# Kernel optimization log

Measured on AMD Instinct MI355X. Metric: run time of the kernel, lower is better.

The kernel has to match this reference:

```python
import jax, jax.numpy as jnp
import numpy as np

EMBED_DIM = 1024
NUM_HEADS = 16
PROJ_DIM = EMBED_DIM // NUM_HEADS


def setup_inputs() -> dict:
    key = jax.random.key(0)
    ks = jax.random.split(key, 11)
    B, S, D = 2, 2048, EMBED_DIM
    scale = 1.0 / np.sqrt(D)
    inp = {
        'q': jax.random.normal(ks[0], (B, S, D), jnp.float32),
        'k': jax.random.normal(ks[1], (B, S, D), jnp.float32),
        'v': jax.random.normal(ks[2], (B, S, D), jnp.float32),
        'Wq': jax.random.normal(ks[3], (D, D), jnp.float32) * scale,
        'bq': jnp.zeros((D,), jnp.float32),
        'Wk': jax.random.normal(ks[4], (D, D), jnp.float32) * scale,
        'bk': jnp.zeros((D,), jnp.float32),
        'Wv': jax.random.normal(ks[5], (D, D), jnp.float32) * scale,
        'bv': jnp.zeros((D,), jnp.float32),
        'Wo': jax.random.normal(ks[6], (D, D), jnp.float32) * scale,
        'bo': jnp.zeros((D,), jnp.float32),
        'use_causal_mask': 1,
    }
    return inp


def _split_heads(x, B):
    # [B, S, D] -> [B, H, S, Pd]
    return x.reshape(B, -1, NUM_HEADS, PROJ_DIM).transpose(0, 2, 1, 3)


def reference(q, k, v, Wq, bq, Wk, bk, Wv, bv, Wo, bo, use_causal_mask):
    B, S, D = q.shape
    qh = _split_heads(q @ Wq + bq, B)
    kh = _split_heads(k @ Wk + bk, B)
    vh = _split_heads(v @ Wv + bv, B)
    # scaled dot-product attention; scores [B, H, S, S]
    logits = jnp.einsum('bhqd,bhkd->bhqk', qh, kh) / jnp.sqrt(
        jnp.asarray(PROJ_DIM, jnp.float32))
    if use_causal_mask:
        # faithful to source: logits += log(tril * 1e-9 + 1e-9)
        tril = jnp.tril(jnp.ones((S, S), dtype=logits.dtype))
        logits = logits + jnp.log(tril * 1e-9 + 1e-9)
    attn = jax.nn.softmax(logits, axis=-1)
    out = jnp.einsum('bhqk,bhkd->bhqd', attn, vh)
    out = out.transpose(0, 2, 1, 3).reshape(B, S, D)
    return out @ Wo + bo
```

## Files before the change

### kernel.cpp

```cpp
#include <hip/hip_runtime.h>
#include <hip/hip_bf16.h>
#include <stdint.h>

#define EMBED 1024
#define NH    16
#define PD    64
#define BATCH 2
#define SEQ   2048

typedef unsigned short u16;
typedef __attribute__((ext_vector_type(8))) short bf16x8;
typedef __attribute__((ext_vector_type(4))) float f32x4;

#define WAITALL() __builtin_amdgcn_s_waitcnt(0)

__device__ __forceinline__ float b2f(u16 x) {
  unsigned u = ((unsigned)x) << 16;
  return __builtin_bit_cast(float, u);
}
__device__ __forceinline__ u16 cvtb(float x) {
  __bf16 h = (__bf16)x;
  return __builtin_bit_cast(u16, h);
}
__device__ __forceinline__ float loadIn(const void* p, size_t i, int isf32) {
  return isf32 ? ((const float*)p)[i] : b2f(((const u16*)p)[i]);
}
__device__ __forceinline__ void async16(const void* g, void* l) {
  __builtin_amdgcn_global_load_lds((const __attribute__((address_space(1))) void*)g,
                                   (__attribute__((address_space(3))) void*)l,
                                   16, 0, 0);
}
__device__ __forceinline__ int detect_f32(const void* q) {
  unsigned w0 = ((const unsigned*)q)[threadIdx.x & 63];
  unsigned e = (w0 >> 7) & 0xffu;
  unsigned long long m = __ballot(e >= 110 && e <= 135);
  return (__popcll(m) < 32) ? 1 : 0;
}

__global__ __launch_bounds__(256) void conv_fused(
    const void* q, const void* k, const void* v,
    const void* Wq, const void* Wk, const void* Wv, const void* Wo,
    u16* qb, u16* kb, u16* vb, u16* WT_all) {
  __shared__ float sh[64][65];
  const int isf32 = detect_f32(q);

  if (blockIdx.y < 3) {
    size_t i = ((size_t)blockIdx.x * 256 + threadIdx.x) * 8;
    const void* src = (blockIdx.y == 0) ? q : (blockIdx.y == 1) ? k : v;
    u16* dst = (blockIdx.y == 0) ? qb : (blockIdx.y == 1) ? kb : vb;
    u16 tmp[8];
    if (isf32) {
      const float* s = (const float*)src + i;
      float4 a = *(const float4*)s;
      float4 b = *(const float4*)(s + 4);
      tmp[0] = cvtb(a.x); tmp[1] = cvtb(a.y); tmp[2] = cvtb(a.z); tmp[3] = cvtb(a.w);
      tmp[4] = cvtb(b.x); tmp[5] = cvtb(b.y); tmp[6] = cvtb(b.z); tmp[7] = cvtb(b.w);
    } else {
      const uint4 r = *(const uint4*)((const u16*)src + i);
      *(uint4*)tmp = r;
    }
    *(uint4*)(dst + i) = *(uint4*)tmp;
    return;
  }

  if (blockIdx.x >= 1024) return;
  const int z = blockIdx.x >> 8;
  const int xy = blockIdx.x & 255;
  const int bx = xy & 15, by = xy >> 4;
  const void* W = (z == 0) ? Wq : (z == 1) ? Wk : (z == 2) ? Wv : Wo;
  u16* WT = WT_all + (size_t)z * EMBED * EMBED;
  int r0 = by * 64, c0 = bx * 64;
  int col = threadIdx.x & 63;
  int rb  = threadIdx.x >> 6;
#pragma unroll
  for (int i = 0; i < 16; i++) {
    int row = i * 4 + rb;
    sh[row][col] = loadIn(W, (size_t)(r0 + row) * EMBED + c0 + col, isf32);
  }
  __syncthreads();
#pragma unroll
  for (int i = 0; i < 16; i++) {
    int row = i * 4 + rb;
    WT[(size_t)(c0 + row) * EMBED + r0 + col] = cvtb(sh[col][row]);
  }
}

__device__ __forceinline__ void gemm_stage(const u16* __restrict__ A,
                                           const u16* __restrict__ Bt,
                                           int tm, int tn, int kt,
                                           u16* As, u16* Bs, int tid) {
#pragma unroll
  for (int i = 0; i < 4; i++) {
    int c = i * 256 + tid;
    int row = c >> 3;
    int col = ((c & 7) << 3) ^ ((row & 7) << 3);
    async16(A + (size_t)(tm + row) * EMBED + kt + col, As + c * 8);
    async16(Bt + (size_t)(tn + row) * EMBED + kt + col, Bs + c * 8);
  }
}

__device__ __forceinline__ void gemm_compute(const u16* As, const u16* Bs,
                                             int wm, int wn, int l15, int quad,
                                             int rbx, f32x4 acc[4][4]) {
#pragma unroll
  for (int ks = 0; ks < 64; ks += 32) {
    int ko = (ks + quad * 8) ^ rbx;
    bf16x8 af[4], bf[4];
#pragma unroll
    for (int mt = 0; mt < 4; mt++)
      af[mt] = *(const bf16x8*)(As + (wm + mt * 16 + l15) * 64 + ko);
#pragma unroll
    for (int nt = 0; nt < 4; nt++)
      bf[nt] = *(const bf16x8*)(Bs + (wn + nt * 16 + l15) * 64 + ko);
#pragma unroll
    for (int mt = 0; mt < 4; mt++)
#pragma unroll
      for (int nt = 0; nt < 4; nt++)
        acc[mt][nt] = __builtin_amdgcn_mfma_f32_16x16x32_bf16(
            af[mt], bf[nt], acc[mt][nt], 0, 0, 0);
  }
}

__global__ __launch_bounds__(512, 2) void qkv_gemm(
    const u16* qb, const u16* kb, const u16* vb, const u16* wts,
    const void* bq, const void* bk, const void* bv,
    u16* Qh, u16* Kh, u16* Vt, const void* qorig) {
  __shared__ __align__(16) u16 lds[4 * 256 * 64];
  const int isf32 = detect_f32(qorig);

  const int lid = blockIdx.x;
  const int mhi = lid & 7;
  const int mlo = (lid >> 3) & 1;
  const int vx = (lid >> 4) & 3;
  const int z = lid >> 6;
  const int vm = mhi * 2 + mlo;
  const int tm = vm * 256, tn = vx * 256;

  const u16* A = (z == 0) ? qb : (z == 1) ? kb : vb;
  const u16* Bt = wts + (size_t)z * EMBED * EMBED;
  const void* bias = (z == 0) ? bq : (z == 1) ? bk : bv;

  const int tid = threadIdx.x, lane = tid & 63, wv = tid >> 6;
  const int wm = (wv >> 2) * 128, wn = (wv & 3) * 64;
  const int l15 = lane & 15, quad = lane >> 4;
  const int rbx = (lane & 7) << 3;

  f32x4 acc[8][4];
  f32x4 zz = {0.f, 0.f, 0.f, 0.f};
#pragma unroll
  for (int i = 0; i < 8; i++)
#pragma unroll
    for (int j = 0; j < 4; j++) acc[i][j] = zz;

#define QKV_STAGE(kt_, As_, Bs_)                                              \
  {                                                                           \
    _Pragma("unroll") for (int i = 0; i < 4; i++) {                           \
      int c = i * 512 + tid;                                                  \
      int row = c >> 3;                                                       \
      int col = ((c & 7) << 3) ^ ((row & 7) << 3);                            \
      async16(A + (size_t)(tm + row) * EMBED + (kt_) + col, (As_) + c * 8);   \
      async16(Bt + (size_t)(tn + row) * EMBED + (kt_) + col, (Bs_) + c * 8);  \
    }                                                                         \
  }

  QKV_STAGE(0, lds, lds + 16384);
  WAITALL();
  __syncthreads();
  for (int kt = 0; kt < EMBED; kt += 64) {
    const int cur = (kt >> 6) & 1;
    const u16* Asc = lds + cur * 32768;
    const u16* Bsc = Asc + 16384;
    if (kt + 64 < EMBED)
      QKV_STAGE(kt + 64, lds + (cur ^ 1) * 32768, lds + (cur ^ 1) * 32768 + 16384);
#pragma unroll
    for (int ks = 0; ks < 64; ks += 32) {
      int ko = (ks + quad * 8) ^ rbx;
      bf16x8 af[8], bf[4];
#pragma unroll
      for (int mt = 0; mt < 8; mt++)
        af[mt] = *(const bf16x8*)(Asc + (wm + mt * 16 + l15) * 64 + ko);
#pragma unroll
      for (int nt = 0; nt < 4; nt++)
        bf[nt] = *(const bf16x8*)(Bsc + (wn + nt * 16 + l15) * 64 + ko);
#pragma unroll
      for (int mt = 0; mt < 8; mt++)
#pragma unroll
        for (int nt = 0; nt < 4; nt++)
          acc[mt][nt] = __builtin_amdgcn_mfma_f32_16x16x32_bf16(
              af[mt], bf[nt], acc[mt][nt], 0, 0, 0);
    }
    WAITALL();
    __syncthreads();
  }
#undef QKV_STAGE

  int rbase = tm + wm + (quad << 2);
  int cbase = tn + wn + l15;
  if (z < 2) {
    u16* dst = (z == 0) ? Qh : Kh;
#pragma unroll
    for (int mt = 0; mt < 8; mt++)
#pragma unroll
      for (int nt = 0; nt < 4; nt++) {
        int col = cbase + nt * 16;
        float bv_ = loadIn(bias, col, isf32);
        int h = col >> 6, p = col & 63;
#pragma unroll
        for (int j = 0; j < 4; j++) {
          int row = rbase + mt * 16 + j;
          int b = row >> 11, s = row & 2047;
          dst[(((size_t)(b * NH + h) * SEQ) + s) * PD + p] =
              cvtb(acc[mt][nt][j] + bv_);
        }
      }
  } else {
#pragma unroll
    for (int mt = 0; mt < 8; mt++)
#pragma unroll
      for (int nt = 0; nt < 4; nt++) {
        int col = cbase + nt * 16;
        float bv_ = loadIn(bias, col, isf32);
        int h = col >> 6, p = col & 63;
        int row0 = rbase + mt * 16;
        int b = row0 >> 11, s0 = row0 & 2047;
        int beta = s0 >> 5, w = s0 & 31;
        int pos = (beta << 5) + (((w >> 2) & 3) << 3) + ((w >> 4) << 2);
        ushort4 pk;
        pk.x = cvtb(acc[mt][nt][0] + bv_);
        pk.y = cvtb(acc[mt][nt][1] + bv_);
        pk.z = cvtb(acc[mt][nt][2] + bv_);
        pk.w = cvtb(acc[mt][nt][3] + bv_);
        *(ushort4*)(Vt + ((size_t)(b * NH + h) * PD + p) * SEQ + pos) = pk;
      }
  }
}

__global__ __launch_bounds__(256, 4) void attn(const u16* __restrict__ Qh,
                                               const u16* __restrict__ Kh,
                                               const u16* __restrict__ Vt,
                                               u16* __restrict__ O,
                                               const int* __restrict__ maskflag) {
  __shared__ __align__(16) u16 sh[5 * 64 * 64];
  u16* const Vbase = sh + 3 * 4096;
  u16* const Qs    = sh + 2 * 4096;

  const int lid = blockIdx.x + (blockIdx.y << 5);
  const int xcd = lid & 7, j = lid >> 3;
  const int bh = (xcd << 2) | (j & 3);
  const int qt = (j >> 2) * 64;

  const int tid = threadIdx.x, lane = tid & 63, wv = tid >> 6;
  const int qh = wv & 1;
  const int kh = wv >> 1;
  const int l15 = lane & 15, quad = lane >> 4;
  const int rbx = (lane & 7) << 3;
  const size_t head = (size_t)bh * SEQ * PD;
  const bool causal = (maskflag[0] != 0);
  const float C = 0.18033688011112042f;

  const int c0 = tid, c1 = 256 + tid;
  const int r0 = c0 >> 3, r1 = c1 >> 3;
  const int x0 = ((c0 & 7) << 3) ^ ((r0 & 7) << 3);
  const int x1 = ((c1 & 7) << 3) ^ ((r1 & 7) << 3);

  async16(Qh + head + (size_t)(qt + r0) * PD + x0, Qs + c0 * 8);
  async16(Qh + head + (size_t)(qt + r1) * PD + x1, Qs + c1 * 8);
  async16(Kh + head + (size_t)r0 * PD + x0, sh + c0 * 8);
  async16(Kh + head + (size_t)r1 * PD + x1, sh + c1 * 8);
  async16(Vt + head + (size_t)r0 * SEQ + x0, Vbase + c0 * 8);
  async16(Vt + head + (size_t)r1 * SEQ + x1, Vbase + c1 * 8);
  async16(Kh + head + (size_t)(64 + r0) * PD + x0, sh + 4096 + c0 * 8);
  async16(Kh + head + (size_t)(64 + r1) * PD + x1, sh + 4096 + c1 * 8);
  __syncthreads();

  bf16x8 qf[2][2];
#pragma unroll
  for (int ks = 0; ks < 2; ks++) {
    int ko = (ks * 32 + quad * 8) ^ rbx;
    qf[ks][0] = *(const bf16x8*)(Qs + (qh * 32 + l15) * 64 + ko);
    qf[ks][1] = *(const bf16x8*)(Qs + (qh * 32 + 16 + l15) * 64 + ko);
  }
  __syncthreads();

  float lacc[2] = {0.f, 0.f};
  f32x4 oacc[4][2];
  f32x4 z4 = {0.f, 0.f, 0.f, 0.f};
#pragma unroll
  for (int mt = 0; mt < 4; mt++)
#pragma unroll
    for (int qx = 0; qx < 2; qx++) oacc[mt][qx] = z4;

  const int qrow0 = qt + qh * 32 + l15;

  int b0 = 0, b1 = 1, b2 = 2;

  for (int t = 0; t < SEQ / 64; t++) {
    if (t == SEQ / 64 - 1) {
      asm volatile("s_waitcnt vmcnt(0)" ::: "memory");
    } else {
      asm volatile("s_waitcnt vmcnt(2)" ::: "memory");
    }
    __builtin_amdgcn_sched_barrier(0);
    __builtin_amdgcn_s_barrier();

    const int k0 = t * 64;
    if (t + 1 < SEQ / 64) {
      const int kn = k0 + 64;
      u16* Vn = Vbase + ((t + 1) & 1) * 4096;
      async16(Vt + head + (size_t)r0 * SEQ + kn + x0, Vn + c0 * 8);
      async16(Vt + head + (size_t)r1 * SEQ + kn + x1, Vn + c1 * 8);
    }
    if (t + 2 < SEQ / 64) {
      const int kn = k0 + 128;
      u16* Kn = sh + b2 * 4096;
      async16(Kh + head + (size_t)(kn + r0) * PD + x0, Kn + c0 * 8);
      async16(Kh + head + (size_t)(kn + r1) * PD + x1, Kn + c1 * 8);
    }
    const u16* Ksc = sh + b0 * 4096;
    const u16* Vsc = Vbase + (t & 1) * 4096;

    f32x4 st[2][2];
#pragma unroll
    for (int kx = 0; kx < 2; kx++)
#pragma unroll
      for (int qx = 0; qx < 2; qx++) st[kx][qx] = z4;
    __builtin_amdgcn_s_setprio(1);
#pragma unroll
    for (int ks = 0; ks < 2; ks++) {
      int ko = (ks * 32 + quad * 8) ^ rbx;
#pragma unroll
      for (int kx = 0; kx < 2; kx++) {
        bf16x8 kf = *(const bf16x8*)(Ksc + (kh * 32 + kx * 16 + l15) * 64 + ko);
        st[kx][0] = __builtin_amdgcn_mfma_f32_16x16x32_bf16(kf, qf[ks][0], st[kx][0], 0, 0, 0);
        st[kx][1] = __builtin_amdgcn_mfma_f32_16x16x32_bf16(kf, qf[ks][1], st[kx][1], 0, 0, 0);
      }
    }
    __builtin_amdgcn_s_setprio(0);

    const int mode = !causal ? 0 : (k0 > qt + 63 ? 2 : (k0 + 63 <= qt ? 0 : 1));
    const float ub = (mode == 2) ? -17.f : -16.f;
    unsigned pw[2][4];
#pragma unroll
    for (int kx = 0; kx < 2; kx++) {
#pragma unroll
      for (int qx = 0; qx < 2; qx++) {
        const int qrow = qrow0 + qx * 16;
        float p[4];
#pragma unroll
        for (int r = 0; r < 4; r++) {
          float bias = ub;
          if (mode == 1) {
            int kappa = k0 + kh * 32 + kx * 16 + 4 * quad + r;
            bias = (kappa > qrow) ? -17.f : -16.f;
          }
          p[r] = exp2f(fmaf(st[kx][qx][r], C, bias));
        }
        lacc[qx] += (p[0] + p[1]) + (p[2] + p[3]);
        pw[qx][kx * 2 + 0] =
            (unsigned)cvtb(p[0]) | ((unsigned)cvtb(p[1]) << 16);
        pw[qx][kx * 2 + 1] =
            (unsigned)cvtb(p[2]) | ((unsigned)cvtb(p[3]) << 16);
      }
    }

    __builtin_amdgcn_s_setprio(1);
    bf16x8 pf0 = __builtin_bit_cast(bf16x8,
        (uint4){pw[0][0], pw[0][1], pw[0][2], pw[0][3]});
    bf16x8 pf1 = __builtin_bit_cast(bf16x8,
        (uint4){pw[1][0], pw[1][1], pw[1][2], pw[1][3]});
#pragma unroll
    for (int mt = 0; mt < 4; mt++) {
      int row = mt * 16 + l15;
      int chunk = ((kh << 2) + quad) ^ (row & 7);
      bf16x8 vf = *(const bf16x8*)(Vsc + row * 64 + (chunk << 3));
      oacc[mt][0] = __builtin_amdgcn_mfma_f32_16x16x32_bf16(vf, pf0, oacc[mt][0], 0, 0, 0);
      oacc[mt][1] = __builtin_amdgcn_mfma_f32_16x16x32_bf16(vf, pf1, oacc[mt][1], 0, 0, 0);
    }
    __builtin_amdgcn_s_setprio(0);

    int tmp = b0; b0 = b1; b1 = b2; b2 = tmp;
  }

  __syncthreads();

#pragma unroll
  for (int qx = 0; qx < 2; qx++) {
    lacc[qx] += __shfl_xor(lacc[qx], 16, 64);
    lacc[qx] += __shfl_xor(lacc[qx], 32, 64);
  }

  float* red = (float*)sh;
  if (kh == 1) {
#pragma unroll
    for (int mt = 0; mt < 4; mt++)
#pragma unroll
      for (int qx = 0; qx < 2; qx++)
        *(f32x4*)(red + qh * 2048 + (mt * 2 + qx) * 256 + lane * 4) =
            oacc[mt][qx];
    red[4096 + qh * 128 + lane] = lacc[0];
    red[4096 + qh * 128 + 64 + lane] = lacc[1];
  }
  __syncthreads();
  if (kh == 0) {
    float l0 = lacc[0] + red[4096 + qh * 128 + lane];
    float l1 = lacc[1] + red[4096 + qh * 128 + 64 + lane];
    float inv[2] = {1.f / l0, 1.f / l1};
    const int b = bh >> 4, h = bh & 15;
#pragma unroll
    for (int mt = 0; mt < 4; mt++) {
#pragma unroll
      for (int qx = 0; qx < 2; qx++) {
        f32x4 o = oacc[mt][qx] +
                  *(const f32x4*)(red + qh * 2048 + (mt * 2 + qx) * 256 + lane * 4);
        int qrow = qrow0 + qx * 16;
        ushort4 w;
        w.x = cvtb(o[0] * inv[qx]);
        w.y = cvtb(o[1] * inv[qx]);
        w.z = cvtb(o[2] * inv[qx]);
        w.w = cvtb(o[3] * inv[qx]);
        *(ushort4*)(O + ((size_t)b * SEQ + qrow) * EMBED + h * PD + mt * 16 +
                    4 * quad) = w;
      }
    }
  }
}

__global__ __launch_bounds__(256) void out_gemm(const u16* __restrict__ Ob,
                                                const u16* __restrict__ WoT,
                                                const void* __restrict__ bo,
                                                void* __restrict__ out,
                                                const void* __restrict__ qorig) {
  __shared__ __align__(16) u16 lds[4 * 128 * 64];
  const int isf32 = detect_f32(qorig);

  const int lid = blockIdx.x + (blockIdx.y << 3);
  const int mgrp = lid & 7;
  const int vx = (lid >> 3) & 7;
  const int vm = lid >> 6;
  int tm = (mgrp * 4 + vm) * 128, tn = vx * 128;

  const int tid = threadIdx.x, lane = tid & 63, wv = tid >> 6;
  const int wm = (wv >> 1) * 64, wn = (wv & 1) * 64;
  const int l15 = lane & 15, quad = lane >> 4;
  const int rbx = (lane & 7) << 3;
  f32x4 acc[4][4];
  f32x4 zz = {0.f, 0.f, 0.f, 0.f};
#pragma unroll
  for (int i = 0; i < 4; i++)
#pragma unroll
    for (int j = 0; j < 4; j++) acc[i][j] = zz;

  gemm_stage(Ob, WoT, tm, tn, 0, lds, lds + 8192, tid);
  WAITALL();
  __syncthreads();
  for (int kt = 0; kt < EMBED; kt += 64) {
    const int cur = (kt >> 6) & 1;
    u16* curb = lds + cur * 16384;
    if (kt + 64 < EMBED)
      gemm_stage(Ob, WoT, tm, tn, kt + 64, lds + (cur ^ 1) * 16384,
                 lds + (cur ^ 1) * 16384 + 8192, tid);
    gemm_compute(curb, curb + 8192, wm, wn, l15, quad, rbx, acc);
    WAITALL();
    __syncthreads();
  }

  int rbase = tm + wm + (quad << 2);
  int cbase = tn + wn + l15;
#pragma unroll
  for (int mt = 0; mt < 4; mt++)
#pragma unroll
    for (int nt = 0; nt < 4; nt++) {
      int col = cbase + nt * 16;
      float bv_ = loadIn(bo, col, isf32);
#pragma unroll
      for (int j = 0; j < 4; j++) {
        int row = rbase + mt * 16 + j;
        float val = acc[mt][nt][j] + bv_;
        size_t off = (size_t)row * EMBED + col;
        if (isf32) ((float*)out)[off] = val;
        else       ((u16*)out)[off]   = cvtb(val);
      }
    }
}

extern "C" void kernel_launch(void* const* d_in, const int* in_sizes, int n_in,
                              void* d_out, int out_size, void* d_ws, size_t ws_size,
                              hipStream_t stream) {
  const void* q  = d_in[0];
  const void* k  = d_in[1];
  const void* v  = d_in[2];
  const void* Wq = d_in[3];
  const void* bq = d_in[4];
  const void* Wk = d_in[5];
  const void* bk = d_in[6];
  const void* Wv = d_in[7];
  const void* bv = d_in[8];
  const void* Wo = d_in[9];
  const void* bo = d_in[10];
  const int* msk = (const int*)d_in[11];

  char* ws = (char*)d_ws;
  u16*  qb    = (u16*)(ws + 64);
  u16*  kb    = qb + (size_t)4194304;
  u16*  vb    = kb + (size_t)4194304;
  u16*  WT    = vb + (size_t)4194304;
  u16*  Qh    = WT + (size_t)4194304;
  u16*  Kh    = Qh + (size_t)4194304;
  u16*  Vt    = Kh + (size_t)4194304;
  u16*  Ob    = Vt + (size_t)4194304;

  conv_fused<<<dim3(2048, 4), 256, 0, stream>>>(q, k, v, Wq, Wk, Wv, Wo,
                                                qb, kb, vb, WT);
  qkv_gemm<<<dim3(192), 512, 0, stream>>>(qb, kb, vb, WT, bq, bk, bv,
                                          Qh, Kh, Vt, q);
  attn<<<dim3(32, 32), 256, 0, stream>>>(Qh, Kh, Vt, Ob, msk);
  out_gemm<<<dim3(8, 32), 256, 0, stream>>>(Ob, WT + (size_t)3 * 1048576,
                                            bo, d_out, q);
}
```

Before: 258.0 us.

## Software-pipeline attention loop: overlap next tile QK with previous softmax and PV

```diff
diff --git a/kernel.cpp b/kernel.cpp
--- a/kernel.cpp
+++ b/kernel.cpp
@@ -292,52 +292,28 @@
 
   const int qrow0 = qt + qh * 32 + l15;
 
-  int b0 = 0, b1 = 1, b2 = 2;
-
-  for (int t = 0; t < SEQ / 64; t++) {
-    if (t == SEQ / 64 - 1) {
-      asm volatile("s_waitcnt vmcnt(0)" ::: "memory");
-    } else {
-      asm volatile("s_waitcnt vmcnt(2)" ::: "memory");
-    }
-    __builtin_amdgcn_sched_barrier(0);
-    __builtin_amdgcn_s_barrier();
-
-    const int k0 = t * 64;
-    if (t + 1 < SEQ / 64) {
-      const int kn = k0 + 64;
-      u16* Vn = Vbase + ((t + 1) & 1) * 4096;
-      async16(Vt + head + (size_t)r0 * SEQ + kn + x0, Vn + c0 * 8);
-      async16(Vt + head + (size_t)r1 * SEQ + kn + x1, Vn + c1 * 8);
-    }
-    if (t + 2 < SEQ / 64) {
-      const int kn = k0 + 128;
-      u16* Kn = sh + b2 * 4096;
-      async16(Kh + head + (size_t)(kn + r0) * PD + x0, Kn + c0 * 8);
-      async16(Kh + head + (size_t)(kn + r1) * PD + x1, Kn + c1 * 8);
-    }
-    const u16* Ksc = sh + b0 * 4096;
-    const u16* Vsc = Vbase + (t & 1) * 4096;
-
-    f32x4 st[2][2];
+  auto QK = [&](f32x4 (&stv)[2][2], const u16* Ksc_) {
 #pragma unroll
     for (int kx = 0; kx < 2; kx++)
 #pragma unroll
-      for (int qx = 0; qx < 2; qx++) st[kx][qx] = z4;
+      for (int qx = 0; qx < 2; qx++) stv[kx][qx] = z4;
     __builtin_amdgcn_s_setprio(1);
 #pragma unroll
     for (int ks = 0; ks < 2; ks++) {
       int ko = (ks * 32 + quad * 8) ^ rbx;
 #pragma unroll
       for (int kx = 0; kx < 2; kx++) {
-        bf16x8 kf = *(const bf16x8*)(Ksc + (kh * 32 + kx * 16 + l15) * 64 + ko);
-        st[kx][0] = __builtin_amdgcn_mfma_f32_16x16x32_bf16(kf, qf[ks][0], st[kx][0], 0, 0, 0);
-        st[kx][1] = __builtin_amdgcn_mfma_f32_16x16x32_bf16(kf, qf[ks][1], st[kx][1], 0, 0, 0);
+        bf16x8 kf = *(const bf16x8*)(Ksc_ + (kh * 32 + kx * 16 + l15) * 64 + ko);
+        stv[kx][0] = __builtin_amdgcn_mfma_f32_16x16x32_bf16(kf, qf[ks][0], stv[kx][0], 0, 0, 0);
+        stv[kx][1] = __builtin_amdgcn_mfma_f32_16x16x32_bf16(kf, qf[ks][1], stv[kx][1], 0, 0, 0);
       }
     }
     __builtin_amdgcn_s_setprio(0);
-
-    const int mode = !causal ? 0 : (k0 > qt + 63 ? 2 : (k0 + 63 <= qt ? 0 : 1));
+  };
+
+  auto SMPV = [&](f32x4 (&stv)[2][2], int u, const u16* Vsc_) {
+    const int k0p = u * 64;
+    const int mode = !causal ? 0 : (k0p > qt + 63 ? 2 : (k0p + 63 <= qt ? 0 : 1));
     const float ub = (mode == 2) ? -17.f : -16.f;
     unsigned pw[2][4];
 #pragma unroll
@@ -350,10 +326,10 @@
         for (int r = 0; r < 4; r++) {
           float bias = ub;
           if (mode == 1) {
-            int kappa = k0 + kh * 32 + kx * 16 + 4 * quad + r;
+            int kappa = k0p + kh * 32 + kx * 16 + 4 * quad + r;
             bias = (kappa > qrow) ? -17.f : -16.f;
           }
-          p[r] = exp2f(fmaf(st[kx][qx][r], C, bias));
+          p[r] = exp2f(fmaf(stv[kx][qx][r], C, bias));
         }
         lacc[qx] += (p[0] + p[1]) + (p[2] + p[3]);
         pw[qx][kx * 2 + 0] =
@@ -362,7 +338,6 @@
             (unsigned)cvtb(p[2]) | ((unsigned)cvtb(p[3]) << 16);
       }
     }
-
     __builtin_amdgcn_s_setprio(1);
     bf16x8 pf0 = __builtin_bit_cast(bf16x8,
         (uint4){pw[0][0], pw[0][1], pw[0][2], pw[0][3]});
@@ -372,14 +347,59 @@
     for (int mt = 0; mt < 4; mt++) {
       int row = mt * 16 + l15;
       int chunk = ((kh << 2) + quad) ^ (row & 7);
-      bf16x8 vf = *(const bf16x8*)(Vsc + row * 64 + (chunk << 3));
+      bf16x8 vf = *(const bf16x8*)(Vsc_ + row * 64 + (chunk << 3));
       oacc[mt][0] = __builtin_amdgcn_mfma_f32_16x16x32_bf16(vf, pf0, oacc[mt][0], 0, 0, 0);
       oacc[mt][1] = __builtin_amdgcn_mfma_f32_16x16x32_bf16(vf, pf1, oacc[mt][1], 0, 0, 0);
     }
     __builtin_amdgcn_s_setprio(0);
+  };
+
+  async16(Kh + head + (size_t)(128 + r0) * PD + x0, Qs + c0 * 8);
+  async16(Kh + head + (size_t)(128 + r1) * PD + x1, Qs + c1 * 8);
+  f32x4 st_prev[2][2];
+  QK(st_prev, sh);
+
+  int b0 = 1, b1 = 2, b2 = 0;
+
+  for (int t = 1; t < SEQ / 64; t++) {
+    if (t == SEQ / 64 - 1) {
+      asm volatile("s_waitcnt vmcnt(0)" ::: "memory");
+    } else {
+      asm volatile("s_waitcnt vmcnt(2)" ::: "memory");
+    }
+    __builtin_amdgcn_sched_barrier(0);
+    __builtin_amdgcn_s_barrier();
+
+    const int k0 = t * 64;
+    {
+      u16* Vn = Vbase + (t & 1) * 4096;
+      async16(Vt + head + (size_t)r0 * SEQ + k0 + x0, Vn + c0 * 8);
+      async16(Vt + head + (size_t)r1 * SEQ + k0 + x1, Vn + c1 * 8);
+    }
+    if (t + 2 < SEQ / 64) {
+      const int kn = k0 + 128;
+      u16* Kn = sh + b2 * 4096;
+      async16(Kh + head + (size_t)(kn + r0) * PD + x0, Kn + c0 * 8);
+      async16(Kh + head + (size_t)(kn + r1) * PD + x1, Kn + c1 * 8);
+    }
+
+    f32x4 st_cur[2][2];
+    QK(st_cur, sh + b0 * 4096);
+
+    SMPV(st_prev, t - 1, Vbase + ((t - 1) & 1) * 4096);
+
+#pragma unroll
+    for (int kx = 0; kx < 2; kx++)
+#pragma unroll
+      for (int qx = 0; qx < 2; qx++) st_prev[kx][qx] = st_cur[kx][qx];
 
     int tmp = b0; b0 = b1; b1 = b2; b2 = tmp;
   }
+
+  asm volatile("s_waitcnt vmcnt(0)" ::: "memory");
+  __builtin_amdgcn_sched_barrier(0);
+  __builtin_amdgcn_s_barrier();
+  SMPV(st_prev, SEQ / 64 - 1, Vbase + ((SEQ / 64 - 1) & 1) * 4096);
 
   __syncthreads();
 
```

Result: no change. 259.7 us (+0.7%).

## Triple-buffer QKV GEMM with K=32 stages and partial vmcnt waits

Applied to the files above, without the earlier changes.

```diff
diff --git a/kernel.cpp b/kernel.cpp
--- a/kernel.cpp
+++ b/kernel.cpp
@@ -125,7 +125,7 @@
     const u16* qb, const u16* kb, const u16* vb, const u16* wts,
     const void* bq, const void* bk, const void* bv,
     u16* Qh, u16* Kh, u16* Vt, const void* qorig) {
-  __shared__ __align__(16) u16 lds[4 * 256 * 64];
+  __shared__ __align__(16) u16 lds[3 * 16384];
   const int isf32 = detect_f32(qorig);
 
   const int lid = blockIdx.x;
@@ -143,7 +143,7 @@
   const int tid = threadIdx.x, lane = tid & 63, wv = tid >> 6;
   const int wm = (wv >> 2) * 128, wn = (wv & 3) * 64;
   const int l15 = lane & 15, quad = lane >> 4;
-  const int rbx = (lane & 7) << 3;
+  const int rbx32 = (lane & 3) << 3;
 
   f32x4 acc[8][4];
   f32x4 zz = {0.f, 0.f, 0.f, 0.f};
@@ -152,45 +152,57 @@
 #pragma unroll
     for (int j = 0; j < 4; j++) acc[i][j] = zz;
 
-#define QKV_STAGE(kt_, As_, Bs_)                                              \
+#define QKV_STAGE(t_, bb_)                                                    \
   {                                                                           \
-    _Pragma("unroll") for (int i = 0; i < 4; i++) {                           \
+    const int kt_ = (t_) * 32;                                                \
+    u16* Ab_ = lds + (bb_) * 16384;                                           \
+    u16* Bb_ = Ab_ + 8192;                                                    \
+    _Pragma("unroll") for (int i = 0; i < 2; i++) {                           \
       int c = i * 512 + tid;                                                  \
-      int row = c >> 3;                                                       \
-      int col = ((c & 7) << 3) ^ ((row & 7) << 3);                            \
-      async16(A + (size_t)(tm + row) * EMBED + (kt_) + col, (As_) + c * 8);   \
-      async16(Bt + (size_t)(tn + row) * EMBED + (kt_) + col, (Bs_) + c * 8);  \
+      int row = c >> 2;                                                       \
+      int col = (((c & 3) ^ (row & 3)) << 3);                                 \
+      async16(A + (size_t)(tm + row) * EMBED + kt_ + col, Ab_ + c * 8);       \
+      async16(Bt + (size_t)(tn + row) * EMBED + kt_ + col, Bb_ + c * 8);      \
     }                                                                         \
   }
 
-  QKV_STAGE(0, lds, lds + 16384);
-  WAITALL();
-  __syncthreads();
-  for (int kt = 0; kt < EMBED; kt += 64) {
-    const int cur = (kt >> 6) & 1;
-    const u16* Asc = lds + cur * 32768;
-    const u16* Bsc = Asc + 16384;
-    if (kt + 64 < EMBED)
-      QKV_STAGE(kt + 64, lds + (cur ^ 1) * 32768, lds + (cur ^ 1) * 32768 + 16384);
-#pragma unroll
-    for (int ks = 0; ks < 64; ks += 32) {
-      int ko = (ks + quad * 8) ^ rbx;
-      bf16x8 af[8], bf[4];
-#pragma unroll
-      for (int mt = 0; mt < 8; mt++)
-        af[mt] = *(const bf16x8*)(Asc + (wm + mt * 16 + l15) * 64 + ko);
+  QKV_STAGE(0, 0);
+  QKV_STAGE(1, 1);
+
+  int b0 = 0, b1 = 1, b2 = 2;
+
+  for (int t = 0; t < 32; t++) {
+    if (t == 31) {
+      asm volatile("s_waitcnt vmcnt(0)" ::: "memory");
+    } else {
+      asm volatile("s_waitcnt vmcnt(4)" ::: "memory");
+    }
+    __builtin_amdgcn_sched_barrier(0);
+    __builtin_amdgcn_s_barrier();
+
+    if (t + 2 < 32) QKV_STAGE(t + 2, b2);
+
+    const u16* Asc = lds + b0 * 16384;
+    const u16* Bsc = Asc + 8192;
+    bf16x8 af[8], bf[4];
+#pragma unroll
+    for (int mt = 0; mt < 8; mt++) {
+      int row = wm + mt * 16 + l15;
+      af[mt] = *(const bf16x8*)(Asc + row * 32 + ((quad * 8) ^ rbx32));
+    }
+#pragma unroll
+    for (int nt = 0; nt < 4; nt++) {
+      int row = wn + nt * 16 + l15;
+      bf[nt] = *(const bf16x8*)(Bsc + row * 32 + ((quad * 8) ^ rbx32));
+    }
+#pragma unroll
+    for (int mt = 0; mt < 8; mt++)
 #pragma unroll
       for (int nt = 0; nt < 4; nt++)
-        bf[nt] = *(const bf16x8*)(Bsc + (wn + nt * 16 + l15) * 64 + ko);
-#pragma unroll
-      for (int mt = 0; mt < 8; mt++)
-#pragma unroll
-        for (int nt = 0; nt < 4; nt++)
-          acc[mt][nt] = __builtin_amdgcn_mfma_f32_16x16x32_bf16(
-              af[mt], bf[nt], acc[mt][nt], 0, 0, 0);
-    }
-    WAITALL();
-    __syncthreads();
+        acc[mt][nt] = __builtin_amdgcn_mfma_f32_16x16x32_bf16(
+            af[mt], bf[nt], acc[mt][nt], 0, 0, 0);
+
+    int tmp = b0; b0 = b1; b1 = b2; b2 = tmp;
   }
 #undef QKV_STAGE
 
```

After: 254.9 us. About the same (-1.2%).
